# Kernel tuning notes

Measured on AMD Instinct MI355X. Metric: run time of the kernel, lower is better.

Reference implementation:

```python
import jax, jax.numpy as jnp
import numpy as np

B, H, W, C = 8, 64, 64, 256
NUM_HEADS = 8
DILATION = 3
KERNEL = 3  # unfold_kernel_size


def setup_inputs() -> dict:
    key = jax.random.key(0)
    k1, k2 = jax.random.split(key)
    x = jax.random.normal(k1, (B, H, W, C), dtype=jnp.float32)
    # torch nn.Linear(dim, 3*dim, bias=False): weight shape [3C, C], y = x @ W.T
    W_qkv = jax.random.normal(k2, (3 * C, C), dtype=jnp.float32) * 0.02
    return {"x": x, "W_qkv": W_qkv}


def _unfold(t, kernel, dilation):
    """nn.Unfold(kernel, dilation, padding=dilation*(3-1)//2, stride=1).
    t: [B, C, H, W] -> [B, C, kernel*kernel, H, W] with (kh, kw) flattened
    in the same order as torch's unfold channel layout (C, kh, kw)."""
    b, c, h, w = t.shape
    p = dilation * (3 - 1) // 2  # hard-coded 3 in source, independent of kernel
    tp = jnp.pad(t, ((0, 0), (0, 0), (p, p), (p, p)))
    pats = [tp[:, :, i * dilation:i * dilation + h, j * dilation:j * dilation + w]
            for i in range(kernel) for j in range(kernel)]
    return jnp.stack(pats, axis=2)  # [B, C, K2, H, W]


def reference(x, W_qkv):
    b, h, w, c = x.shape
    dph = c // NUM_HEADS  # dim per head
    scale = dph ** -0.5
    k2 = KERNEL * KERNEL
    # qkv linear, split as (3, c) on last dim -> [3, b, c, h, w]
    qkv = jnp.einsum('bhwc,oc->bhwo', x, W_qkv).reshape(b, h, w, 3, c)
    qkv = jnp.transpose(qkv, (3, 0, 4, 1, 2))
    q, k, v = qkv[0], qkv[1], qkv[2]  # each [b, c, h, w]
    # unfold k, v into dilated local windows: [b, heads, dph, k2, n]
    k = _unfold(k, KERNEL, DILATION).reshape(b, NUM_HEADS, dph, k2, h * w)
    v = _unfold(v, KERNEL, DILATION).reshape(b, NUM_HEADS, dph, k2, h * w)
    q = q.reshape(b, NUM_HEADS, dph, h * w)
    # per-pixel 1xdph @ dphxk2 attention scores
    attn = jnp.einsum('bndm,bndkm->bnmk', q, k) * scale  # [b, heads, n, k2]
    attn = jax.nn.softmax(attn, axis=-1)
    out = jnp.einsum('bnmk,bndkm->bnmd', attn, v)  # [b, heads, n, dph]
    # rearrange 'b nh (h w) 1 d -> b h w (nh 1 d)'
    out = jnp.transpose(out, (0, 2, 1, 3)).reshape(b, h, w, c)
    return out
```

## Files before the change

### kernel.cpp

```cpp
#include <hip/hip_runtime.h>
#include <hip/hip_bf16.h>


typedef unsigned short ushortT;
typedef __attribute__((ext_vector_type(8))) short short8;
typedef __attribute__((ext_vector_type(4))) float f32x4;

__device__ __forceinline__ ushortT f2b(float f) {
    unsigned u = __float_as_uint(f);
    return (ushortT)((u + 0x7fffu + ((u >> 16) & 1u)) >> 16);
}
__device__ __forceinline__ float b2f(ushortT u) {
    return __uint_as_float((unsigned)u << 16);
}

__global__ __launch_bounds__(256) void to_bf16(const float* __restrict__ x,
                                               const float* __restrict__ wq,
                                               ushortT* __restrict__ xb,
                                               ushortT* __restrict__ wb) {
    const int N4X = 2097152, N4W = 49152;
    int i = blockIdx.x * 256 + threadIdx.x;
    if (i < N4X) {
        float4 f = ((const float4*)x)[i];
        ushort4 u = {f2b(f.x), f2b(f.y), f2b(f.z), f2b(f.w)};
        ((ushort4*)xb)[i] = u;
    } else {
        int j = i - N4X;
        if (j < N4W) {
            float4 f = ((const float4*)wq)[j];
            ushort4 u = {f2b(f.x), f2b(f.y), f2b(f.z), f2b(f.w)};
            ((ushort4*)wb)[j] = u;
        }
    }
}

__global__ __launch_bounds__(256) void gemm_qkv(const ushortT* __restrict__ A,
                                                const ushortT* __restrict__ Bw,
                                                ushortT* __restrict__ Y) {
    __shared__ __align__(16) ushortT smem[16384];
    ushortT* As = smem;
    ushortT* Bs = smem + 8192;

    int bid = blockIdx.x;
    int swz = (bid & 7) * 192 + (bid >> 3);
    int mblk = swz / 6, nblk = swz - mblk * 6;
    const int m0 = mblk * 128, n0 = nblk * 128;

    const int t = threadIdx.x;
    const int lane = t & 63, wv = t >> 6;
    const int wm = (wv >> 1) * 64, wn = (wv & 1) * 64;
    const int lr = lane & 15, g = lane >> 4;
    const int srow = t >> 3, sslot = t & 7;
    const int wvbase = (t & ~63) * 8;

    f32x4 acc[4][4] = {};

    for (int k0 = 0; k0 < 256; k0 += 64) {
        __syncthreads();
#pragma unroll
        for (int r = 0; r < 4; ++r) {
            int row = r * 32 + srow;
            int ss = sslot ^ (row & 7);
            const ushortT* ga = A + (size_t)(m0 + row) * 256 + k0 + ss * 8;
            const ushortT* gb = Bw + (size_t)(n0 + row) * 256 + k0 + ss * 8;
            __builtin_amdgcn_global_load_lds(
                (const __attribute__((address_space(1))) unsigned int*)ga,
                (__attribute__((address_space(3))) unsigned int*)(As + r * 2048 + wvbase),
                16, 0, 0);
            __builtin_amdgcn_global_load_lds(
                (const __attribute__((address_space(1))) unsigned int*)gb,
                (__attribute__((address_space(3))) unsigned int*)(Bs + r * 2048 + wvbase),
                16, 0, 0);
        }
        __syncthreads();

#pragma unroll
        for (int ksub = 0; ksub < 2; ++ksub) {
            short8 af[4], bfr[4];
#pragma unroll
            for (int mi = 0; mi < 4; ++mi) {
                int row = wm + mi * 16 + lr;
                int slot = (ksub * 4 + g) ^ (row & 7);
                af[mi] = *(const short8*)&As[row * 64 + slot * 8];
            }
#pragma unroll
            for (int ni = 0; ni < 4; ++ni) {
                int row = wn + ni * 16 + lr;
                int slot = (ksub * 4 + g) ^ (row & 7);
                bfr[ni] = *(const short8*)&Bs[row * 64 + slot * 8];
            }
#pragma unroll
            for (int mi = 0; mi < 4; ++mi)
#pragma unroll
                for (int ni = 0; ni < 4; ++ni)
                    acc[mi][ni] = __builtin_amdgcn_mfma_f32_16x16x32_bf16(
                        af[mi], bfr[ni], acc[mi][ni], 0, 0, 0);
        }
    }

    __syncthreads();
#pragma unroll
    for (int mi = 0; mi < 4; ++mi)
#pragma unroll
        for (int ni = 0; ni < 4; ++ni) {
            int col = wn + ni * 16 + lr;
#pragma unroll
            for (int rg = 0; rg < 4; ++rg) {
                int row = wm + mi * 16 + g * 4 + rg;
                int sc = col ^ (((row >> 2) & 3) << 4);
                smem[row * 128 + sc] = f2b(acc[mi][ni][rg]);
            }
        }
    __syncthreads();
#pragma unroll
    for (int p = 0; p < 8; ++p) {
        int cid = p * 256 + t;
        int row = cid >> 4;
        int c0 = (cid & 15) * 8;
        int sc0 = c0 ^ (((row >> 2) & 3) << 4);
        short8 vv = *(const short8*)&smem[row * 128 + sc0];
        *(short8*)&Y[(size_t)(m0 + row) * 768 + n0 + c0] = vv;
    }
}

__global__ __launch_bounds__(256) void attn3(const ushortT* __restrict__ qkv,
                                             float* __restrict__ out) {
    const float scale = 0.17677669529663689f;
    int bid = blockIdx.x;
    int sbid = (bid & 7) * 512 + (bid >> 3);
    const int t = threadIdx.x;
    const int wpair = sbid * 4 + (t >> 6);
    const int half = (t >> 5) & 1;
    const int l = t & 31;
    const int wid = wpair * 2 + half;
    const int b = wid >> 12, pix = wid & 4095;
    const int h = pix >> 6, w = pix & 63;

    const size_t pbase = (size_t)wid * 768;
    short8 qu = *(const short8*)&qkv[pbase + l * 8];
    float q[8];
#pragma unroll
    for (int c = 0; c < 8; ++c) q[c] = b2f((ushortT)qu[c]) * scale;

    float s[9];
    short8 vu[9];
#pragma unroll
    for (int i = 0; i < 3; ++i) {
#pragma unroll
        for (int j = 0; j < 3; ++j) {
            const int kk = i * 3 + j;
            const int hh = h + (i - 1) * 3;
            const int ww = w + (j - 1) * 3;
            float p = 0.f;
            short8 z = {0, 0, 0, 0, 0, 0, 0, 0};
            vu[kk] = z;
            if ((unsigned)hh < 64u && (unsigned)ww < 64u) {
                const size_t nb = ((size_t)((b << 12) + (hh << 6) + ww)) * 768;
                short8 ku = *(const short8*)&qkv[nb + 256 + l * 8];
                vu[kk] = *(const short8*)&qkv[nb + 512 + l * 8];
#pragma unroll
                for (int c = 0; c < 8; ++c) p = fmaf(q[c], b2f((ushortT)ku[c]), p);
            }
            p += __shfl_xor(p, 1);
            p += __shfl_xor(p, 2);
            s[kk] = p;
        }
    }

    float m = s[0];
#pragma unroll
    for (int kk = 1; kk < 9; ++kk) m = fmaxf(m, s[kk]);
    float denom = 0.f;
    float o[8] = {};
#pragma unroll
    for (int kk = 0; kk < 9; ++kk) {
        float e = __expf(s[kk] - m);
        denom += e;
#pragma unroll
        for (int c = 0; c < 8; ++c) o[c] = fmaf(e, b2f((ushortT)vu[kk][c]), o[c]);
    }
    const float inv = 1.0f / denom;
    float* op = &out[(size_t)wid * 256 + l * 8];
    float4 o0 = make_float4(o[0] * inv, o[1] * inv, o[2] * inv, o[3] * inv);
    float4 o1 = make_float4(o[4] * inv, o[5] * inv, o[6] * inv, o[7] * inv);
    *(float4*)op = o0;
    *(float4*)(op + 4) = o1;
}

extern "C" void kernel_launch(void* const* d_in, const int* in_sizes, int n_in,
                              void* d_out, int out_size, void* d_ws, size_t ws_size,
                              hipStream_t stream) {
    const float* x  = (const float*)d_in[0];
    const float* Wq = (const float*)d_in[1];
    float* out = (float*)d_out;

    ushortT* xb  = (ushortT*)d_ws;
    ushortT* wb  = xb + (size_t)8388608;
    ushortT* qkv = wb + (size_t)196608;

    to_bf16<<<8384, 256, 0, stream>>>(x, Wq, xb, wb);
    gemm_qkv<<<1536, 256, 0, stream>>>(xb, wb, qkv);
    attn3<<<4096, 256, 0, stream>>>(qkv, out);
}
```

Before: 52.52 us.

## Fuse fp32-to-bf16 conversion of x into the QKV GEMM A-tile load

Drops the separate pass that converts x to bf16. The GEMM now loads fp32 x tiles straight into LDS with an XOR swizzle and converts them to packed bf16 using v_cvt_pk_bf16_f32 when building MFMA fragments. This removes a full write and re-read of the bf16 copy of x, about 16MB of fp32 reads plus 16MB of bf16 traffic. In exchange, every GEMM block reads fp32 A, which doubles A load bytes. A is re-read by the six n-blocks and the LDS footprint grows, which may reduce occupancy.

```diff
diff --git a/kernel.cpp b/kernel.cpp
--- a/kernel.cpp
+++ b/kernel.cpp
@@ -5,6 +5,7 @@
 typedef unsigned short ushortT;
 typedef __attribute__((ext_vector_type(8))) short short8;
 typedef __attribute__((ext_vector_type(4))) float f32x4;
+typedef __attribute__((ext_vector_type(4))) unsigned int u32x4;
 
 __device__ __forceinline__ ushortT f2b(float f) {
     unsigned u = __float_as_uint(f);
@@ -13,33 +14,26 @@
 __device__ __forceinline__ float b2f(ushortT u) {
     return __uint_as_float((unsigned)u << 16);
 }
-
-__global__ __launch_bounds__(256) void to_bf16(const float* __restrict__ x,
-                                               const float* __restrict__ wq,
-                                               ushortT* __restrict__ xb,
-                                               ushortT* __restrict__ wb) {
-    const int N4X = 2097152, N4W = 49152;
+__device__ __forceinline__ unsigned cvtpk(float a, float b) {
+    unsigned r;
+    asm("v_cvt_pk_bf16_f32 %0, %1, %2" : "=v"(r) : "v"(a), "v"(b));
+    return r;
+}
+
+__global__ __launch_bounds__(256) void wcvt(const float* __restrict__ wq,
+                                            ushortT* __restrict__ wb) {
     int i = blockIdx.x * 256 + threadIdx.x;
-    if (i < N4X) {
-        float4 f = ((const float4*)x)[i];
-        ushort4 u = {f2b(f.x), f2b(f.y), f2b(f.z), f2b(f.w)};
-        ((ushort4*)xb)[i] = u;
-    } else {
-        int j = i - N4X;
-        if (j < N4W) {
-            float4 f = ((const float4*)wq)[j];
-            ushort4 u = {f2b(f.x), f2b(f.y), f2b(f.z), f2b(f.w)};
-            ((ushort4*)wb)[j] = u;
-        }
-    }
-}
-
-__global__ __launch_bounds__(256) void gemm_qkv(const ushortT* __restrict__ A,
+    float4 f = ((const float4*)wq)[i];
+    ushort4 u = {f2b(f.x), f2b(f.y), f2b(f.z), f2b(f.w)};
+    ((ushort4*)wb)[i] = u;
+}
+
+__global__ __launch_bounds__(256) void gemm_qkv(const float* __restrict__ A,
                                                 const ushortT* __restrict__ Bw,
                                                 ushortT* __restrict__ Y) {
-    __shared__ __align__(16) ushortT smem[16384];
-    ushortT* As = smem;
-    ushortT* Bs = smem + 8192;
+    __shared__ __align__(16) ushortT smem[24576];
+    float* Af = (float*)smem;
+    ushortT* Bs = smem + 16384;
 
     int bid = blockIdx.x;
     int swz = (bid & 7) * 192 + (bid >> 3);
@@ -51,22 +45,28 @@
     const int wm = (wv >> 1) * 64, wn = (wv & 1) * 64;
     const int lr = lane & 15, g = lane >> 4;
     const int srow = t >> 3, sslot = t & 7;
+    const int arow = t >> 4, aslot = t & 15;
     const int wvbase = (t & ~63) * 8;
 
     f32x4 acc[4][4] = {};
 
     for (int k0 = 0; k0 < 256; k0 += 64) {
         __syncthreads();
+#pragma unroll
+        for (int p = 0; p < 8; ++p) {
+            int row = p * 16 + arow;
+            int ss = aslot ^ (row & 15);
+            const float* ga = A + (size_t)(m0 + row) * 256 + k0 + ss * 4;
+            __builtin_amdgcn_global_load_lds(
+                (const __attribute__((address_space(1))) unsigned int*)ga,
+                (__attribute__((address_space(3))) unsigned int*)(smem + p * 2048 + wvbase),
+                16, 0, 0);
+        }
 #pragma unroll
         for (int r = 0; r < 4; ++r) {
             int row = r * 32 + srow;
             int ss = sslot ^ (row & 7);
-            const ushortT* ga = A + (size_t)(m0 + row) * 256 + k0 + ss * 8;
             const ushortT* gb = Bw + (size_t)(n0 + row) * 256 + k0 + ss * 8;
-            __builtin_amdgcn_global_load_lds(
-                (const __attribute__((address_space(1))) unsigned int*)ga,
-                (__attribute__((address_space(3))) unsigned int*)(As + r * 2048 + wvbase),
-                16, 0, 0);
             __builtin_amdgcn_global_load_lds(
                 (const __attribute__((address_space(1))) unsigned int*)gb,
                 (__attribute__((address_space(3))) unsigned int*)(Bs + r * 2048 + wvbase),
@@ -80,8 +80,17 @@
 #pragma unroll
             for (int mi = 0; mi < 4; ++mi) {
                 int row = wm + mi * 16 + lr;
-                int slot = (ksub * 4 + g) ^ (row & 7);
-                af[mi] = *(const short8*)&As[row * 64 + slot * 8];
+                int jb = 2 * (ksub * 4 + g);
+                int s0 = jb ^ (row & 15);
+                int s1 = (jb + 1) ^ (row & 15);
+                f32x4 lo = *(const f32x4*)&Af[row * 64 + s0 * 4];
+                f32x4 hi = *(const f32x4*)&Af[row * 64 + s1 * 4];
+                u32x4 pk;
+                pk[0] = cvtpk(lo[0], lo[1]);
+                pk[1] = cvtpk(lo[2], lo[3]);
+                pk[2] = cvtpk(hi[0], hi[1]);
+                pk[3] = cvtpk(hi[2], hi[3]);
+                af[mi] = __builtin_bit_cast(short8, pk);
             }
 #pragma unroll
             for (int ni = 0; ni < 4; ++ni) {
@@ -194,11 +203,10 @@
     const float* Wq = (const float*)d_in[1];
     float* out = (float*)d_out;
 
-    ushortT* xb  = (ushortT*)d_ws;
-    ushortT* wb  = xb + (size_t)8388608;
+    ushortT* wb  = (ushortT*)d_ws;
     ushortT* qkv = wb + (size_t)196608;
 
-    to_bf16<<<8384, 256, 0, stream>>>(x, Wq, xb, wb);
-    gemm_qkv<<<1536, 256, 0, stream>>>(xb, wb, qkv);
+    wcvt<<<192, 256, 0, stream>>>(Wq, wb);
+    gemm_qkv<<<1536, 256, 0, stream>>>(x, wb, qkv);
     attn3<<<4096, 256, 0, stream>>>(qkv, out);
 }
```

New measurement: 55.55 us. +5.8%, slower.

## Double-buffer GEMM LDS tiles with K=32 stages to overlap loads and MFMA

Applied to the files above, without the earlier changes.

Restructures the QKV GEMM main loop from four K=64 single-buffered stages into eight K=32 stages that alternate between two LDS buffers, so the async global-to-LDS load of the next stage is issued before the current stage's MFMAs run. It also changes the XOR swizzle to suit the 32-element row width. The intent is to hide global load latency behind compute and remove one barrier per stage. The cost is twice as many stage iterations, each with less MFMA work per barrier.

```diff
diff --git a/kernel.cpp b/kernel.cpp
--- a/kernel.cpp
+++ b/kernel.cpp
@@ -38,8 +38,6 @@
                                                 const ushortT* __restrict__ Bw,
                                                 ushortT* __restrict__ Y) {
     __shared__ __align__(16) ushortT smem[16384];
-    ushortT* As = smem;
-    ushortT* Bs = smem + 8192;
 
     int bid = blockIdx.x;
     int swz = (bid & 7) * 192 + (bid >> 3);
@@ -50,55 +48,63 @@
     const int lane = t & 63, wv = t >> 6;
     const int wm = (wv >> 1) * 64, wn = (wv & 1) * 64;
     const int lr = lane & 15, g = lane >> 4;
-    const int srow = t >> 3, sslot = t & 7;
-    const int wvbase = (t & ~63) * 8;
+    const int srow = t >> 2, sslot = t & 3;
+    const int wvb = (t & ~63) * 8;
 
     f32x4 acc[4][4] = {};
 
-    for (int k0 = 0; k0 < 256; k0 += 64) {
+#define STAGE(bo, k0)                                                                 \
+    do {                                                                              \
+        _Pragma("unroll")                                                             \
+        for (int p = 0; p < 2; ++p) {                                                 \
+            int row = p * 64 + srow;                                                  \
+            int ss = sslot ^ ((row >> 1) & 3);                                        \
+            const ushortT* ga = A + (size_t)(m0 + row) * 256 + (k0) + ss * 8;         \
+            __builtin_amdgcn_global_load_lds(                                         \
+                (const __attribute__((address_space(1))) unsigned int*)ga,            \
+                (__attribute__((address_space(3))) unsigned int*)(smem + (bo) + p * 2048 + wvb), \
+                16, 0, 0);                                                            \
+            const ushortT* gb = Bw + (size_t)(n0 + row) * 256 + (k0) + ss * 8;        \
+            __builtin_amdgcn_global_load_lds(                                         \
+                (const __attribute__((address_space(1))) unsigned int*)gb,            \
+                (__attribute__((address_space(3))) unsigned int*)(smem + (bo) + 4096 + p * 2048 + wvb), \
+                16, 0, 0);                                                            \
+        }                                                                             \
+    } while (0)
+
+    STAGE(0, 0);
+    __syncthreads();
+
+#pragma unroll
+    for (int ks = 0; ks < 8; ++ks) {
+        const int cur = (ks & 1) * 8192;
+        const int nxt = 8192 - cur;
+        if (ks < 7) STAGE(nxt, (ks + 1) * 32);
+
+        short8 af[4], bfr[4];
+#pragma unroll
+        for (int mi = 0; mi < 4; ++mi) {
+            int row = wm + mi * 16 + lr;
+            int slot = g ^ ((row >> 1) & 3);
+            af[mi] = *(const short8*)&smem[cur + row * 32 + slot * 8];
+        }
+#pragma unroll
+        for (int ni = 0; ni < 4; ++ni) {
+            int row = wn + ni * 16 + lr;
+            int slot = g ^ ((row >> 1) & 3);
+            bfr[ni] = *(const short8*)&smem[cur + 4096 + row * 32 + slot * 8];
+        }
+#pragma unroll
+        for (int mi = 0; mi < 4; ++mi)
+#pragma unroll
+            for (int ni = 0; ni < 4; ++ni)
+                acc[mi][ni] = __builtin_amdgcn_mfma_f32_16x16x32_bf16(
+                    af[mi], bfr[ni], acc[mi][ni], 0, 0, 0);
+
         __syncthreads();
-#pragma unroll
-        for (int r = 0; r < 4; ++r) {
-            int row = r * 32 + srow;
-            int ss = sslot ^ (row & 7);
-            const ushortT* ga = A + (size_t)(m0 + row) * 256 + k0 + ss * 8;
-            const ushortT* gb = Bw + (size_t)(n0 + row) * 256 + k0 + ss * 8;
-            __builtin_amdgcn_global_load_lds(
-                (const __attribute__((address_space(1))) unsigned int*)ga,
-                (__attribute__((address_space(3))) unsigned int*)(As + r * 2048 + wvbase),
-                16, 0, 0);
-            __builtin_amdgcn_global_load_lds(
-                (const __attribute__((address_space(1))) unsigned int*)gb,
-                (__attribute__((address_space(3))) unsigned int*)(Bs + r * 2048 + wvbase),
-                16, 0, 0);
-        }
-        __syncthreads();
-
-#pragma unroll
-        for (int ksub = 0; ksub < 2; ++ksub) {
-            short8 af[4], bfr[4];
-#pragma unroll
-            for (int mi = 0; mi < 4; ++mi) {
-                int row = wm + mi * 16 + lr;
-                int slot = (ksub * 4 + g) ^ (row & 7);
-                af[mi] = *(const short8*)&As[row * 64 + slot * 8];
-            }
-#pragma unroll
-            for (int ni = 0; ni < 4; ++ni) {
-                int row = wn + ni * 16 + lr;
-                int slot = (ksub * 4 + g) ^ (row & 7);
-                bfr[ni] = *(const short8*)&Bs[row * 64 + slot * 8];
-            }
-#pragma unroll
-            for (int mi = 0; mi < 4; ++mi)
-#pragma unroll
-                for (int ni = 0; ni < 4; ++ni)
-                    acc[mi][ni] = __builtin_amdgcn_mfma_f32_16x16x32_bf16(
-                        af[mi], bfr[ni], acc[mi][ni], 0, 0, 0);
-        }
-    }
-
-    __syncthreads();
+    }
+#undef STAGE
+
 #pragma unroll
     for (int mi = 0; mi < 4; ++mi)
 #pragma unroll
```

Result: slower. 55.68 us (+6.0%).

## Load GEMM B operand directly to registers and halve LDS footprint

Applied to the files above, without the earlier changes.

The QKV GEMM now loads its weight (B) fragments straight from global memory into registers, with the first k-half prefetched before the barrier and the second half loaded after it. Only the activation tile A is staged in LDS, which halves shared memory per block so more blocks can be resident on each CU. The epilogue writes the output tile through LDS in two 64-row halves to fit the smaller buffer. In exchange, each wave does uncoalesced 16-byte global loads of B rows, which are duplicated across the waves that share a column band, raises register pressure, and adds an extra barrier in the epilogue.

```diff
diff --git a/kernel.cpp b/kernel.cpp
--- a/kernel.cpp
+++ b/kernel.cpp
@@ -37,9 +37,7 @@
 __global__ __launch_bounds__(256) void gemm_qkv(const ushortT* __restrict__ A,
                                                 const ushortT* __restrict__ Bw,
                                                 ushortT* __restrict__ Y) {
-    __shared__ __align__(16) ushortT smem[16384];
-    ushortT* As = smem;
-    ushortT* Bs = smem + 8192;
+    __shared__ __align__(16) ushortT smem[8192];
 
     int bid = blockIdx.x;
     int swz = (bid & 7) * 192 + (bid >> 3);
@@ -53,73 +51,84 @@
     const int srow = t >> 3, sslot = t & 7;
     const int wvbase = (t & ~63) * 8;
 
+    const ushortT* browp[4];
+#pragma unroll
+    for (int ni = 0; ni < 4; ++ni)
+        browp[ni] = Bw + (size_t)(n0 + wn + ni * 16 + lr) * 256;
+
     f32x4 acc[4][4] = {};
 
-    for (int k0 = 0; k0 < 256; k0 += 64) {
+#pragma unroll
+    for (int ks = 0; ks < 4; ++ks) {
+        const int k0 = ks * 64;
+        short8 b0[4], b1[4];
+#pragma unroll
+        for (int ni = 0; ni < 4; ++ni)
+            b0[ni] = *(const short8*)(browp[ni] + k0 + g * 8);
+
         __syncthreads();
 #pragma unroll
         for (int r = 0; r < 4; ++r) {
             int row = r * 32 + srow;
             int ss = sslot ^ (row & 7);
             const ushortT* ga = A + (size_t)(m0 + row) * 256 + k0 + ss * 8;
-            const ushortT* gb = Bw + (size_t)(n0 + row) * 256 + k0 + ss * 8;
             __builtin_amdgcn_global_load_lds(
                 (const __attribute__((address_space(1))) unsigned int*)ga,
-                (__attribute__((address_space(3))) unsigned int*)(As + r * 2048 + wvbase),
+                (__attribute__((address_space(3))) unsigned int*)(smem + r * 2048 + wvbase),
                 16, 0, 0);
-            __builtin_amdgcn_global_load_lds(
-                (const __attribute__((address_space(1))) unsigned int*)gb,
-                (__attribute__((address_space(3))) unsigned int*)(Bs + r * 2048 + wvbase),
-                16, 0, 0);
         }
         __syncthreads();
 
 #pragma unroll
+        for (int ni = 0; ni < 4; ++ni)
+            b1[ni] = *(const short8*)(browp[ni] + k0 + 32 + g * 8);
+
+#pragma unroll
         for (int ksub = 0; ksub < 2; ++ksub) {
-            short8 af[4], bfr[4];
+            short8 af[4];
 #pragma unroll
             for (int mi = 0; mi < 4; ++mi) {
                 int row = wm + mi * 16 + lr;
                 int slot = (ksub * 4 + g) ^ (row & 7);
-                af[mi] = *(const short8*)&As[row * 64 + slot * 8];
-            }
-#pragma unroll
-            for (int ni = 0; ni < 4; ++ni) {
-                int row = wn + ni * 16 + lr;
-                int slot = (ksub * 4 + g) ^ (row & 7);
-                bfr[ni] = *(const short8*)&Bs[row * 64 + slot * 8];
+                af[mi] = *(const short8*)&smem[row * 64 + slot * 8];
             }
 #pragma unroll
             for (int mi = 0; mi < 4; ++mi)
 #pragma unroll
                 for (int ni = 0; ni < 4; ++ni)
                     acc[mi][ni] = __builtin_amdgcn_mfma_f32_16x16x32_bf16(
-                        af[mi], bfr[ni], acc[mi][ni], 0, 0, 0);
+                        af[mi], ksub ? b1[ni] : b0[ni], acc[mi][ni], 0, 0, 0);
         }
     }
 
     __syncthreads();
 #pragma unroll
-    for (int mi = 0; mi < 4; ++mi)
-#pragma unroll
-        for (int ni = 0; ni < 4; ++ni) {
-            int col = wn + ni * 16 + lr;
-#pragma unroll
-            for (int rg = 0; rg < 4; ++rg) {
-                int row = wm + mi * 16 + g * 4 + rg;
-                int sc = col ^ (((row >> 2) & 3) << 4);
-                smem[row * 128 + sc] = f2b(acc[mi][ni][rg]);
-            }
-        }
-    __syncthreads();
-#pragma unroll
-    for (int p = 0; p < 8; ++p) {
-        int cid = p * 256 + t;
-        int row = cid >> 4;
-        int c0 = (cid & 15) * 8;
-        int sc0 = c0 ^ (((row >> 2) & 3) << 4);
-        short8 vv = *(const short8*)&smem[row * 128 + sc0];
-        *(short8*)&Y[(size_t)(m0 + row) * 768 + n0 + c0] = vv;
+    for (int hf = 0; hf < 2; ++hf) {
+        if ((wv >> 1) == hf) {
+#pragma unroll
+            for (int mi = 0; mi < 4; ++mi)
+#pragma unroll
+                for (int ni = 0; ni < 4; ++ni) {
+                    int col = wn + ni * 16 + lr;
+#pragma unroll
+                    for (int rg = 0; rg < 4; ++rg) {
+                        int rl = mi * 16 + g * 4 + rg;
+                        int sc = col ^ (((rl >> 2) & 3) << 4);
+                        smem[rl * 128 + sc] = f2b(acc[mi][ni][rg]);
+                    }
+                }
+        }
+        __syncthreads();
+#pragma unroll
+        for (int p = 0; p < 4; ++p) {
+            int cid = p * 256 + t;
+            int row = cid >> 4;
+            int c0 = (cid & 15) * 8;
+            int sc0 = c0 ^ (((row >> 2) & 3) << 4);
+            short8 vv = *(const short8*)&smem[row * 128 + sc0];
+            *(short8*)&Y[(size_t)(m0 + hf * 64 + row) * 768 + n0 + c0] = vv;
+        }
+        if (hf == 0) __syncthreads();
     }
 }
 
```

Measured after the change: 70.13 us. 1.34x slower.
